# Kernel optimization log

Hardware: AMD Instinct MI355X
Metric: run time of the kernel (lower is better)

## Reference

```python
import jax, jax.numpy as jnp
import numpy as np

MODEL_DIM = 1024
NUM_HEADS = 8
DIM_PER_HEAD = MODEL_DIM // NUM_HEADS  # 128
BATCH = 4
NODE_LEN = 128  # must equal DIM_PER_HEAD (see v += relative_mul broadcast in source)
LN_EPS = 1e-5


def setup_inputs() -> dict:
    key0 = jax.random.key(0)
    ks = jax.random.split(key0, 16)
    def w(k, shape, s=0.02):
        return jax.random.normal(k, shape, dtype=jnp.float32) * s
    inp = {
        "key": jax.random.normal(ks[0], (BATCH, NODE_LEN, MODEL_DIM), dtype=jnp.float32),
        "value": jax.random.normal(ks[1], (BATCH, NODE_LEN, MODEL_DIM), dtype=jnp.float32),
        "query": jax.random.normal(ks[2], (BATCH, NODE_LEN, MODEL_DIM), dtype=jnp.float32),
        "relative_q": jax.random.normal(ks[3], (BATCH * NUM_HEADS, NODE_LEN, NODE_LEN, DIM_PER_HEAD), dtype=jnp.float32),
        "relative_v": jax.random.normal(ks[4], (BATCH * NUM_HEADS, NODE_LEN, NODE_LEN, DIM_PER_HEAD), dtype=jnp.float32),
        "Wq": w(ks[5], (MODEL_DIM, MODEL_DIM)), "bq": w(ks[6], (MODEL_DIM,)),
        "Wk": w(ks[7], (MODEL_DIM, MODEL_DIM)), "bk": w(ks[8], (MODEL_DIM,)),
        "Wv": w(ks[9], (MODEL_DIM, MODEL_DIM)), "bv": w(ks[10], (MODEL_DIM,)),
        "Wo": w(ks[11], (MODEL_DIM, MODEL_DIM)), "bo": w(ks[12], (MODEL_DIM,)),
        "ln_gamma": jnp.ones((MODEL_DIM,), dtype=jnp.float32),
        "ln_beta": jnp.zeros((MODEL_DIM,), dtype=jnp.float32),
    }
    return inp


def _relative_mul(x, rel):
    # x: [BH, L, d], rel: [BH, L, L, d] -> [BH, L, L]
    # result[b,i,j] = sum_d x[b,i,d] * rel[b,i,j,d]  (matches torch bmm chain)
    return jnp.einsum('bid,bijd->bij', x, rel)


def reference(key, value, query, relative_q, relative_v,
              Wq, bq, Wk, bk, Wv, bv, Wo, bo, ln_gamma, ln_beta):
    residual = query
    B = key.shape[0]
    H, d = NUM_HEADS, DIM_PER_HEAD

    k = key @ Wk.T + bk      # [B, L, model_dim]
    v = value @ Wv.T + bv
    q = query @ Wq.T + bq

    # faithful to torch .view(batch*heads, -1, dim_per_head): row-major reshape
    k = k.reshape(B * H, -1, d)  # [BH, L, d]
    v = v.reshape(B * H, -1, d)
    q = q.reshape(B * H, -1, d)

    # scale = (dim_per_head // num_heads) ** -0.5, as in source
    scale = (d // H) ** (-0.5)

    attn = jnp.einsum('bid,bjd->bij', q, k)           # [BH, L, L]
    attn = attn + _relative_mul(q, relative_q)
    attn = attn * scale
    attn = jax.nn.softmax(attn, axis=2)

    # source: v += relative_mul(v, relative_v); requires L == d
    v = v + _relative_mul(v, relative_v)              # [BH, L, d] (L == d)
    context = jnp.einsum('bij,bjd->bid', attn, v)     # [BH, L, d]
    context = context.reshape(B, -1, H * d)           # [B, L, model_dim]

    out = context @ Wo.T + bo
    out = out + residual
    mu = jnp.mean(out, axis=-1, keepdims=True)
    var = jnp.mean(jnp.square(out - mu), axis=-1, keepdims=True)
    out = (out - mu) * jax.lax.rsqrt(var + LN_EPS) * ln_gamma + ln_beta
    return (out, attn)
```

## Files before the change

kernel.cpp:

```cpp
#include <hip/hip_runtime.h>

#define MD 1024
#define L 128
#define LN_EPS 1e-5f

typedef __attribute__((ext_vector_type(8))) short bh8;
typedef __attribute__((ext_vector_type(4))) float fx4;
typedef __attribute__((ext_vector_type(4))) float f4;

__device__ __forceinline__ unsigned short f2bf(float x) {
  unsigned int u = __float_as_uint(x);
  u = (u + 0x7FFFu + ((u >> 16) & 1u)) >> 16;
  return (unsigned short)u;
}

__global__ __launch_bounds__(256) void cvt_bf16(
    const float* s0, const float* s1, const float* s2, const float* s3,
    const float* s4, const float* s5, const float* s6, unsigned short* d0,
    unsigned short* d1, unsigned short* d2, unsigned short* d3,
    unsigned short* d4, unsigned short* d5, unsigned short* d6) {
  const float* s;
  unsigned short* d;
  int n;
  switch (blockIdx.z) {
    case 0: s = s0; d = d0; n = 524288; break;
    case 1: s = s1; d = d1; n = 524288; break;
    case 2: s = s2; d = d2; n = 524288; break;
    case 3: s = s3; d = d3; n = 1048576; break;
    case 4: s = s4; d = d4; n = 1048576; break;
    case 5: s = s5; d = d5; n = 1048576; break;
    default: s = s6; d = d6; n = 1048576; break;
  }
  const int idx = (blockIdx.x * 256 + threadIdx.x) * 8;
  if (idx < n) {
    const float4 a = *(const float4*)&s[idx];
    const float4 b = *(const float4*)&s[idx + 4];
    uint4 o;
    o.x = (unsigned int)f2bf(a.x) | ((unsigned int)f2bf(a.y) << 16);
    o.y = (unsigned int)f2bf(a.z) | ((unsigned int)f2bf(a.w) << 16);
    o.z = (unsigned int)f2bf(b.x) | ((unsigned int)f2bf(b.y) << 16);
    o.w = (unsigned int)f2bf(b.z) | ((unsigned int)f2bf(b.w) << 16);
    *(uint4*)&d[idx] = o;
  }
}

__device__ __forceinline__ void mfma_gemm_body(
    const unsigned short* __restrict__ A, const unsigned short* __restrict__ W,
    const float* __restrict__ bias, float* __restrict__ out,
    unsigned short* __restrict__ outb) {
  __shared__ short As[64][40];
  __shared__ short Bs[64][40];
  const int t = threadIdx.x;
  const int row0 = blockIdx.x * 64;
  const int col0 = blockIdx.y * 64;
  const int l = t & 63;
  const int w = t >> 6;
  const int wr = (w >> 1) * 32;
  const int wc = (w & 1) * 32;
  const int srow = t >> 2;
  const int skg = (t & 3) * 8;
  const int fr = l & 15;
  const int fq = (l >> 4) * 8;

  fx4 z = {0.f, 0.f, 0.f, 0.f};
  fx4 acc[2][2];
  acc[0][0] = z; acc[0][1] = z; acc[1][0] = z; acc[1][1] = z;

  for (int k0 = 0; k0 < MD; k0 += 32) {
    const uint4 av = *(const uint4*)&A[(size_t)(row0 + srow) * MD + k0 + skg];
    const uint4 bv = *(const uint4*)&W[(size_t)(col0 + srow) * MD + k0 + skg];
    __syncthreads();
    *(uint4*)&As[srow][skg] = av;
    *(uint4*)&Bs[srow][skg] = bv;
    __syncthreads();
    const bh8 a0 = *(const bh8*)&As[wr + fr][fq];
    const bh8 a1 = *(const bh8*)&As[wr + 16 + fr][fq];
    const bh8 b0 = *(const bh8*)&Bs[wc + fr][fq];
    const bh8 b1 = *(const bh8*)&Bs[wc + 16 + fr][fq];
    acc[0][0] = __builtin_amdgcn_mfma_f32_16x16x32_bf16(a0, b0, acc[0][0], 0, 0, 0);
    acc[0][1] = __builtin_amdgcn_mfma_f32_16x16x32_bf16(a0, b1, acc[0][1], 0, 0, 0);
    acc[1][0] = __builtin_amdgcn_mfma_f32_16x16x32_bf16(a1, b0, acc[1][0], 0, 0, 0);
    acc[1][1] = __builtin_amdgcn_mfma_f32_16x16x32_bf16(a1, b1, acc[1][1], 0, 0, 0);
  }

  const int fq4 = (l >> 4) * 4;
#pragma unroll
  for (int m = 0; m < 2; m++)
#pragma unroll
    for (int n = 0; n < 2; n++) {
      const int col = col0 + wc + n * 16 + fr;
      const float bval = bias[col];
#pragma unroll
      for (int r = 0; r < 4; r++) {
        const int row = row0 + wr + m * 16 + fq4 + r;
        const float v = acc[m][n][r] + bval;
        if (out) out[(size_t)row * MD + col] = v;
        if (outb) outb[(size_t)row * MD + col] = f2bf(v);
      }
    }
}

__global__ __launch_bounds__(256) void qkv_mfma(
    const unsigned short* Aq, const unsigned short* Ak,
    const unsigned short* Av, const unsigned short* Wq,
    const unsigned short* Wk, const unsigned short* Wv, const float* bq,
    const float* bk, const float* bv, float* qo, float* ko, float* vo,
    unsigned short* qb, unsigned short* kb) {
  if (blockIdx.z == 0) mfma_gemm_body(Aq, Wq, bq, qo, qb);
  else if (blockIdx.z == 1) mfma_gemm_body(Ak, Wk, bk, ko, kb);
  else mfma_gemm_body(Av, Wv, bv, vo, nullptr);
}

__global__ __launch_bounds__(256) void o_mfma(const unsigned short* A,
                                              const unsigned short* W,
                                              const float* bias, float* out) {
  mfma_gemm_body(A, W, bias, out, nullptr);
}

__global__ __launch_bounds__(256) void qk_mfma(const unsigned short* __restrict__ qb,
                                               const unsigned short* __restrict__ kb,
                                               float* __restrict__ S1) {
  __shared__ short Qs[128][40];
  __shared__ short Ks[128][40];
  const int g = blockIdx.x;
  const int t = threadIdx.x;
  const int l = t & 63;
  const int w = t >> 6;
  const unsigned short* qg = qb + (size_t)g * 16384;
  const unsigned short* kg = kb + (size_t)g * 16384;
  const int srow = t >> 1;
  const int sh = (t & 1) * 16;
  const int fr = l & 15;
  const int fq = (l >> 4) * 8;

  fx4 z = {0.f, 0.f, 0.f, 0.f};
  fx4 acc[2][8];
#pragma unroll
  for (int m = 0; m < 2; m++)
#pragma unroll
    for (int n = 0; n < 8; n++) acc[m][n] = z;

  for (int d0 = 0; d0 < 128; d0 += 32) {
    const size_t off = (size_t)srow * 128 + d0 + sh;
    const uint4 q0 = *(const uint4*)&qg[off];
    const uint4 q1 = *(const uint4*)&qg[off + 8];
    const uint4 k0 = *(const uint4*)&kg[off];
    const uint4 k1 = *(const uint4*)&kg[off + 8];
    __syncthreads();
    *(uint4*)&Qs[srow][sh] = q0;
    *(uint4*)&Qs[srow][sh + 8] = q1;
    *(uint4*)&Ks[srow][sh] = k0;
    *(uint4*)&Ks[srow][sh + 8] = k1;
    __syncthreads();
    const bh8 a0 = *(const bh8*)&Qs[w * 32 + fr][fq];
    const bh8 a1 = *(const bh8*)&Qs[w * 32 + 16 + fr][fq];
#pragma unroll
    for (int n = 0; n < 8; n++) {
      const bh8 b = *(const bh8*)&Ks[n * 16 + fr][fq];
      acc[0][n] = __builtin_amdgcn_mfma_f32_16x16x32_bf16(a0, b, acc[0][n], 0, 0, 0);
      acc[1][n] = __builtin_amdgcn_mfma_f32_16x16x32_bf16(a1, b, acc[1][n], 0, 0, 0);
    }
  }

  const int fq4 = (l >> 4) * 4;
#pragma unroll
  for (int m = 0; m < 2; m++)
#pragma unroll
    for (int n = 0; n < 8; n++)
#pragma unroll
      for (int r = 0; r < 4; r++) {
        const int i = w * 32 + m * 16 + fq4 + r;
        S1[((size_t)g * 128 + i) * 128 + n * 16 + fr] = acc[m][n][r];
      }
}

__global__ __launch_bounds__(256) void rel_fused(
    const float* __restrict__ q, const float* __restrict__ v,
    const float* __restrict__ rq, const float* __restrict__ rv,
    const float* __restrict__ S1, float* __restrict__ attn,
    float* __restrict__ v2) {
  const int g = blockIdx.x;
  const int i = blockIdx.y;
  const int t = threadIdx.x;
  const int w = t >> 6;
  const int l = t & 63;
  const int c = t & 31;
  const int rlow = t >> 5;

  __shared__ float logits[L];
  __shared__ float vacc_s[L];

  const size_t gi = (size_t)g * L + i;
  const f4 qf = *(const f4*)&q[gi * 128 + c * 4];
  const f4 vf = *(const f4*)&v[gi * 128 + c * 4];

  const f4* rqp = (const f4*)(rq + gi * 16384);
  const f4* rvp = (const f4*)(rv + gi * 16384);

  float aq[16], av[16];
#pragma unroll
  for (int k = 0; k < 16; k++) {
    const f4 d = __builtin_nontemporal_load(&rqp[t + 256 * k]);
    aq[k] = qf.x * d.x + qf.y * d.y + qf.z * d.z + qf.w * d.w;
  }
#pragma unroll
  for (int k = 0; k < 16; k++) {
    const f4 d = __builtin_nontemporal_load(&rvp[t + 256 * k]);
    av[k] = vf.x * d.x + vf.y * d.y + vf.z * d.z + vf.w * d.w;
  }

#pragma unroll
  for (int mask = 1; mask <= 16; mask <<= 1) {
#pragma unroll
    for (int k = 0; k < 16; k++) {
      aq[k] += __shfl_xor(aq[k], mask);
      av[k] += __shfl_xor(av[k], mask);
    }
  }
  if (c == 0) {
#pragma unroll
    for (int k = 0; k < 16; k++) {
      const int row = 8 * k + rlow;
      logits[row] = aq[k];
      vacc_s[row] = av[k];
    }
  }

  __syncthreads();
  if (w == 0) {
    const float* S1p = S1 + gi * 128;
    const float x0 = (logits[l] + S1p[l]) * 0.25f;
    const float x1 = (logits[l + 64] + S1p[l + 64]) * 0.25f;
    float m = fmaxf(x0, x1);
#pragma unroll
    for (int mask = 1; mask <= 32; mask <<= 1) m = fmaxf(m, __shfl_xor(m, mask));
    const float e0 = __expf(x0 - m);
    const float e1 = __expf(x1 - m);
    float ssum = e0 + e1;
#pragma unroll
    for (int mask = 1; mask <= 32; mask <<= 1) ssum += __shfl_xor(ssum, mask);
    const float inv = 1.0f / ssum;
    attn[gi * 128 + l] = e0 * inv;
    attn[gi * 128 + l + 64] = e1 * inv;
  }
  if (t < 128) v2[gi * 128 + t] = v[gi * 128 + t] + vacc_s[t];
}

__global__ __launch_bounds__(256) void context_k(const float* __restrict__ attn,
                                                 const float* __restrict__ v2,
                                                 unsigned short* __restrict__ ctxb) {
  const int g = blockIdx.x;
  const int i = blockIdx.y;
  const int t = threadIdx.x;
  const int dd = t & 127;
  const int h = t >> 7;
  __shared__ float arow[L];
  __shared__ float part[128];
  const size_t gi = (size_t)g * L + i;
  if (t < L) arow[t] = attn[gi * 128 + t];
  __syncthreads();
  float acc = 0.f;
  const float* v2g = v2 + (size_t)g * (L * 128);
#pragma unroll 8
  for (int j = h * 64; j < h * 64 + 64; j++)
    acc = fmaf(arow[j], v2g[j * 128 + dd], acc);
  if (h == 1) part[dd] = acc;
  __syncthreads();
  if (h == 0) ctxb[gi * 128 + dd] = f2bf(acc + part[dd]);
}

__global__ __launch_bounds__(256) void resid_ln(const float* __restrict__ pre,
                                                const float* __restrict__ resid,
                                                const float* __restrict__ gamma,
                                                const float* __restrict__ beta,
                                                float* __restrict__ out) {
  const int r = blockIdx.x;
  const int t = threadIdx.x;
  const float4 p = *(const float4*)&pre[(size_t)r * MD + t * 4];
  const float4 rs = *(const float4*)&resid[(size_t)r * MD + t * 4];
  float4 x;
  x.x = p.x + rs.x; x.y = p.y + rs.y; x.z = p.z + rs.z; x.w = p.w + rs.w;
  float s = x.x + x.y + x.z + x.w;
  float ss = x.x * x.x + x.y * x.y + x.z * x.z + x.w * x.w;
#pragma unroll
  for (int mask = 1; mask <= 32; mask <<= 1) {
    s += __shfl_xor(s, mask);
    ss += __shfl_xor(ss, mask);
  }
  __shared__ float as_[4], aq_[4];
  const int w = t >> 6;
  if ((t & 63) == 0) { as_[w] = s; aq_[w] = ss; }
  __syncthreads();
  s = as_[0] + as_[1] + as_[2] + as_[3];
  ss = aq_[0] + aq_[1] + aq_[2] + aq_[3];
  const float mu = s * (1.0f / 1024.0f);
  const float var = ss * (1.0f / 1024.0f) - mu * mu;
  const float inv = rsqrtf(var + LN_EPS);
  const float4 g4 = *(const float4*)&gamma[t * 4];
  const float4 b4 = *(const float4*)&beta[t * 4];
  float4 o;
  o.x = (x.x - mu) * inv * g4.x + b4.x;
  o.y = (x.y - mu) * inv * g4.y + b4.y;
  o.z = (x.z - mu) * inv * g4.z + b4.z;
  o.w = (x.w - mu) * inv * g4.w + b4.w;
  *(float4*)&out[(size_t)r * MD + t * 4] = o;
}

extern "C" void kernel_launch(void* const* d_in, const int* in_sizes, int n_in,
                              void* d_out, int out_size, void* d_ws,
                              size_t ws_size, hipStream_t stream) {
  (void)in_sizes; (void)n_in; (void)out_size; (void)ws_size;
  const float* key = (const float*)d_in[0];
  const float* value = (const float*)d_in[1];
  const float* query = (const float*)d_in[2];
  const float* rq = (const float*)d_in[3];
  const float* rv = (const float*)d_in[4];
  const float* Wq = (const float*)d_in[5];
  const float* bq = (const float*)d_in[6];
  const float* Wk = (const float*)d_in[7];
  const float* bk = (const float*)d_in[8];
  const float* Wv = (const float*)d_in[9];
  const float* bv = (const float*)d_in[10];
  const float* Wo = (const float*)d_in[11];
  const float* bo = (const float*)d_in[12];
  const float* gamma = (const float*)d_in[13];
  const float* beta = (const float*)d_in[14];

  float* out0 = (float*)d_out;
  float* attn_out = (float*)d_out + 524288;

  float* ws = (float*)d_ws;
  float* q_ws = ws;
  float* k_ws = ws + 524288;
  float* v_ws = ws + 2 * 524288;
  float* v2_ws = ws + 3 * 524288;
  float* pre_ws = ws + 4 * 524288;
  float* S1_ws = ws + 5 * 524288;
  unsigned short* us = (unsigned short*)(ws + 6 * 524288);
  unsigned short* qb = us;
  unsigned short* kb = us + 524288;
  unsigned short* inqb = us + 2 * 524288;
  unsigned short* inkb = us + 3 * 524288;
  unsigned short* invb = us + 4 * 524288;
  unsigned short* ctxb = us + 5 * 524288;
  unsigned short* Wqb = us + 6 * 524288;
  unsigned short* Wkb = Wqb + 1048576;
  unsigned short* Wvb = Wkb + 1048576;
  unsigned short* Wob = Wvb + 1048576;

  cvt_bf16<<<dim3(512, 1, 7), 256, 0, stream>>>(query, key, value, Wq, Wk, Wv,
                                                Wo, inqb, inkb, invb, Wqb, Wkb,
                                                Wvb, Wob);
  qkv_mfma<<<dim3(8, 16, 3), 256, 0, stream>>>(inqb, inkb, invb, Wqb, Wkb, Wvb,
                                               bq, bk, bv, q_ws, k_ws, v_ws,
                                               qb, kb);
  qk_mfma<<<32, 256, 0, stream>>>(qb, kb, S1_ws);
  rel_fused<<<dim3(32, 128), 256, 0, stream>>>(q_ws, v_ws, rq, rv, S1_ws,
                                               attn_out, v2_ws);
  context_k<<<dim3(32, 128), 256, 0, stream>>>(attn_out, v2_ws, ctxb);
  o_mfma<<<dim3(8, 16), 256, 0, stream>>>(ctxb, Wob, bo, pre_ws);
  resid_ln<<<512, 256, 0, stream>>>(pre_ws, query, gamma, beta, out0);
}
```

Baseline: 150.8 us.

## Fuse bf16 conversion into GEMM loads and compute context with MFMA

Removes the separate fp32-to-bf16 conversion kernel by converting inputs and weights on the fly inside the GEMM tile loads. Drops the unused fp32 k output. The attention-times-V product moves from a scalar FMA kernel to a bf16 MFMA kernel; rel_fused now emits a bf16 copy of attn and a transposed bf16 v2. GEMM loads now read twice the bytes per tile, and the context product loses precision in bf16. The new MFMA context kernel launches only 32 blocks, so parallelism is low.

```diff
diff --git a/kernel.cpp b/kernel.cpp
--- a/kernel.cpp
+++ b/kernel.cpp
@@ -14,38 +14,18 @@
   return (unsigned short)u;
 }
 
-__global__ __launch_bounds__(256) void cvt_bf16(
-    const float* s0, const float* s1, const float* s2, const float* s3,
-    const float* s4, const float* s5, const float* s6, unsigned short* d0,
-    unsigned short* d1, unsigned short* d2, unsigned short* d3,
-    unsigned short* d4, unsigned short* d5, unsigned short* d6) {
-  const float* s;
-  unsigned short* d;
-  int n;
-  switch (blockIdx.z) {
-    case 0: s = s0; d = d0; n = 524288; break;
-    case 1: s = s1; d = d1; n = 524288; break;
-    case 2: s = s2; d = d2; n = 524288; break;
-    case 3: s = s3; d = d3; n = 1048576; break;
-    case 4: s = s4; d = d4; n = 1048576; break;
-    case 5: s = s5; d = d5; n = 1048576; break;
-    default: s = s6; d = d6; n = 1048576; break;
-  }
-  const int idx = (blockIdx.x * 256 + threadIdx.x) * 8;
-  if (idx < n) {
-    const float4 a = *(const float4*)&s[idx];
-    const float4 b = *(const float4*)&s[idx + 4];
-    uint4 o;
-    o.x = (unsigned int)f2bf(a.x) | ((unsigned int)f2bf(a.y) << 16);
-    o.y = (unsigned int)f2bf(a.z) | ((unsigned int)f2bf(a.w) << 16);
-    o.z = (unsigned int)f2bf(b.x) | ((unsigned int)f2bf(b.y) << 16);
-    o.w = (unsigned int)f2bf(b.z) | ((unsigned int)f2bf(b.w) << 16);
-    *(uint4*)&d[idx] = o;
-  }
-}
-
+__device__ __forceinline__ uint4 pack8(const float4 a, const float4 b) {
+  uint4 o;
+  o.x = (unsigned int)f2bf(a.x) | ((unsigned int)f2bf(a.y) << 16);
+  o.y = (unsigned int)f2bf(a.z) | ((unsigned int)f2bf(a.w) << 16);
+  o.z = (unsigned int)f2bf(b.x) | ((unsigned int)f2bf(b.y) << 16);
+  o.w = (unsigned int)f2bf(b.z) | ((unsigned int)f2bf(b.w) << 16);
+  return o;
+}
+
+template <int AMODE>
 __device__ __forceinline__ void mfma_gemm_body(
-    const unsigned short* __restrict__ A, const unsigned short* __restrict__ W,
+    const void* __restrict__ Ap, const float* __restrict__ Wf,
     const float* __restrict__ bias, float* __restrict__ out,
     unsigned short* __restrict__ outb) {
   __shared__ short As[64][40];
@@ -67,8 +47,21 @@
   acc[0][0] = z; acc[0][1] = z; acc[1][0] = z; acc[1][1] = z;
 
   for (int k0 = 0; k0 < MD; k0 += 32) {
-    const uint4 av = *(const uint4*)&A[(size_t)(row0 + srow) * MD + k0 + skg];
-    const uint4 bv = *(const uint4*)&W[(size_t)(col0 + srow) * MD + k0 + skg];
+    uint4 av, bv;
+    if (AMODE == 1) {
+      const unsigned short* Ab = (const unsigned short*)Ap;
+      av = *(const uint4*)&Ab[(size_t)(row0 + srow) * MD + k0 + skg];
+    } else {
+      const float* Af = (const float*)Ap;
+      const float4 a0 = *(const float4*)&Af[(size_t)(row0 + srow) * MD + k0 + skg];
+      const float4 a1 = *(const float4*)&Af[(size_t)(row0 + srow) * MD + k0 + skg + 4];
+      av = pack8(a0, a1);
+    }
+    {
+      const float4 b0 = *(const float4*)&Wf[(size_t)(col0 + srow) * MD + k0 + skg];
+      const float4 b1 = *(const float4*)&Wf[(size_t)(col0 + srow) * MD + k0 + skg + 4];
+      bv = pack8(b0, b1);
+    }
     __syncthreads();
     *(uint4*)&As[srow][skg] = av;
     *(uint4*)&Bs[srow][skg] = bv;
@@ -101,20 +94,19 @@
 }
 
 __global__ __launch_bounds__(256) void qkv_mfma(
-    const unsigned short* Aq, const unsigned short* Ak,
-    const unsigned short* Av, const unsigned short* Wq,
-    const unsigned short* Wk, const unsigned short* Wv, const float* bq,
-    const float* bk, const float* bv, float* qo, float* ko, float* vo,
+    const float* query, const float* key, const float* value,
+    const float* Wq, const float* Wk, const float* Wv, const float* bq,
+    const float* bk, const float* bv, float* qo, float* vo,
     unsigned short* qb, unsigned short* kb) {
-  if (blockIdx.z == 0) mfma_gemm_body(Aq, Wq, bq, qo, qb);
-  else if (blockIdx.z == 1) mfma_gemm_body(Ak, Wk, bk, ko, kb);
-  else mfma_gemm_body(Av, Wv, bv, vo, nullptr);
+  if (blockIdx.z == 0) mfma_gemm_body<0>(query, Wq, bq, qo, qb);
+  else if (blockIdx.z == 1) mfma_gemm_body<0>(key, Wk, bk, nullptr, kb);
+  else mfma_gemm_body<0>(value, Wv, bv, vo, nullptr);
 }
 
 __global__ __launch_bounds__(256) void o_mfma(const unsigned short* A,
-                                              const unsigned short* W,
+                                              const float* W,
                                               const float* bias, float* out) {
-  mfma_gemm_body(A, W, bias, out, nullptr);
+  mfma_gemm_body<1>(A, W, bias, out, nullptr);
 }
 
 __global__ __launch_bounds__(256) void qk_mfma(const unsigned short* __restrict__ qb,
@@ -178,7 +170,7 @@
     const float* __restrict__ q, const float* __restrict__ v,
     const float* __restrict__ rq, const float* __restrict__ rv,
     const float* __restrict__ S1, float* __restrict__ attn,
-    float* __restrict__ v2) {
+    unsigned short* __restrict__ attnb, unsigned short* __restrict__ v2tb) {
   const int g = blockIdx.x;
   const int i = blockIdx.y;
   const int t = threadIdx.x;
@@ -240,33 +232,76 @@
 #pragma unroll
     for (int mask = 1; mask <= 32; mask <<= 1) ssum += __shfl_xor(ssum, mask);
     const float inv = 1.0f / ssum;
-    attn[gi * 128 + l] = e0 * inv;
-    attn[gi * 128 + l + 64] = e1 * inv;
-  }
-  if (t < 128) v2[gi * 128 + t] = v[gi * 128 + t] + vacc_s[t];
-}
-
-__global__ __launch_bounds__(256) void context_k(const float* __restrict__ attn,
-                                                 const float* __restrict__ v2,
-                                                 unsigned short* __restrict__ ctxb) {
+    const float a0 = e0 * inv;
+    const float a1 = e1 * inv;
+    attn[gi * 128 + l] = a0;
+    attn[gi * 128 + l + 64] = a1;
+    attnb[gi * 128 + l] = f2bf(a0);
+    attnb[gi * 128 + l + 64] = f2bf(a1);
+  }
+  if (t < 128) {
+    const float val = v[gi * 128 + t] + vacc_s[t];
+    v2tb[(size_t)g * 16384 + (size_t)t * 128 + i] = f2bf(val);
+  }
+}
+
+__global__ __launch_bounds__(256) void ctx_mfma(
+    const unsigned short* __restrict__ attnb,
+    const unsigned short* __restrict__ v2tb,
+    unsigned short* __restrict__ ctxb) {
+  __shared__ short Qs[128][40];
+  __shared__ short Ks[128][40];
   const int g = blockIdx.x;
-  const int i = blockIdx.y;
-  const int t = threadIdx.x;
-  const int dd = t & 127;
-  const int h = t >> 7;
-  __shared__ float arow[L];
-  __shared__ float part[128];
-  const size_t gi = (size_t)g * L + i;
-  if (t < L) arow[t] = attn[gi * 128 + t];
-  __syncthreads();
-  float acc = 0.f;
-  const float* v2g = v2 + (size_t)g * (L * 128);
-#pragma unroll 8
-  for (int j = h * 64; j < h * 64 + 64; j++)
-    acc = fmaf(arow[j], v2g[j * 128 + dd], acc);
-  if (h == 1) part[dd] = acc;
-  __syncthreads();
-  if (h == 0) ctxb[gi * 128 + dd] = f2bf(acc + part[dd]);
+  const int t = threadIdx.x;
+  const int l = t & 63;
+  const int w = t >> 6;
+  const unsigned short* ag = attnb + (size_t)g * 16384;
+  const unsigned short* bg = v2tb + (size_t)g * 16384;
+  const int srow = t >> 1;
+  const int sh = (t & 1) * 16;
+  const int fr = l & 15;
+  const int fq = (l >> 4) * 8;
+
+  fx4 z = {0.f, 0.f, 0.f, 0.f};
+  fx4 acc[2][8];
+#pragma unroll
+  for (int m = 0; m < 2; m++)
+#pragma unroll
+    for (int n = 0; n < 8; n++) acc[m][n] = z;
+
+  for (int j0 = 0; j0 < 128; j0 += 32) {
+    const size_t off = (size_t)srow * 128 + j0 + sh;
+    const uint4 q0 = *(const uint4*)&ag[off];
+    const uint4 q1 = *(const uint4*)&ag[off + 8];
+    const uint4 k0 = *(const uint4*)&bg[off];
+    const uint4 k1 = *(const uint4*)&bg[off + 8];
+    __syncthreads();
+    *(uint4*)&Qs[srow][sh] = q0;
+    *(uint4*)&Qs[srow][sh + 8] = q1;
+    *(uint4*)&Ks[srow][sh] = k0;
+    *(uint4*)&Ks[srow][sh + 8] = k1;
+    __syncthreads();
+    const bh8 a0 = *(const bh8*)&Qs[w * 32 + fr][fq];
+    const bh8 a1 = *(const bh8*)&Qs[w * 32 + 16 + fr][fq];
+#pragma unroll
+    for (int n = 0; n < 8; n++) {
+      const bh8 b = *(const bh8*)&Ks[n * 16 + fr][fq];
+      acc[0][n] = __builtin_amdgcn_mfma_f32_16x16x32_bf16(a0, b, acc[0][n], 0, 0, 0);
+      acc[1][n] = __builtin_amdgcn_mfma_f32_16x16x32_bf16(a1, b, acc[1][n], 0, 0, 0);
+    }
+  }
+
+  const int fq4 = (l >> 4) * 4;
+#pragma unroll
+  for (int m = 0; m < 2; m++)
+#pragma unroll
+    for (int n = 0; n < 8; n++)
+#pragma unroll
+      for (int r = 0; r < 4; r++) {
+        const int i = w * 32 + m * 16 + fq4 + r;
+        ctxb[(size_t)g * 16384 + (size_t)i * 128 + n * 16 + fr] =
+            f2bf(acc[m][n][r]);
+      }
 }
 
 __global__ __launch_bounds__(256) void resid_ln(const float* __restrict__ pre,
@@ -331,33 +366,22 @@
 
   float* ws = (float*)d_ws;
   float* q_ws = ws;
-  float* k_ws = ws + 524288;
-  float* v_ws = ws + 2 * 524288;
-  float* v2_ws = ws + 3 * 524288;
-  float* pre_ws = ws + 4 * 524288;
-  float* S1_ws = ws + 5 * 524288;
-  unsigned short* us = (unsigned short*)(ws + 6 * 524288);
+  float* v_ws = ws + 524288;
+  float* pre_ws = ws + 2 * 524288;
+  float* S1_ws = ws + 3 * 524288;
+  unsigned short* us = (unsigned short*)(ws + 4 * 524288);
   unsigned short* qb = us;
   unsigned short* kb = us + 524288;
-  unsigned short* inqb = us + 2 * 524288;
-  unsigned short* inkb = us + 3 * 524288;
-  unsigned short* invb = us + 4 * 524288;
-  unsigned short* ctxb = us + 5 * 524288;
-  unsigned short* Wqb = us + 6 * 524288;
-  unsigned short* Wkb = Wqb + 1048576;
-  unsigned short* Wvb = Wkb + 1048576;
-  unsigned short* Wob = Wvb + 1048576;
-
-  cvt_bf16<<<dim3(512, 1, 7), 256, 0, stream>>>(query, key, value, Wq, Wk, Wv,
-                                                Wo, inqb, inkb, invb, Wqb, Wkb,
-                                                Wvb, Wob);
-  qkv_mfma<<<dim3(8, 16, 3), 256, 0, stream>>>(inqb, inkb, invb, Wqb, Wkb, Wvb,
-                                               bq, bk, bv, q_ws, k_ws, v_ws,
-                                               qb, kb);
+  unsigned short* attnb = us + 2 * 524288;
+  unsigned short* v2tb = us + 3 * 524288;
+  unsigned short* ctxb = us + 4 * 524288;
+
+  qkv_mfma<<<dim3(8, 16, 3), 256, 0, stream>>>(query, key, value, Wq, Wk, Wv,
+                                               bq, bk, bv, q_ws, v_ws, qb, kb);
   qk_mfma<<<32, 256, 0, stream>>>(qb, kb, S1_ws);
   rel_fused<<<dim3(32, 128), 256, 0, stream>>>(q_ws, v_ws, rq, rv, S1_ws,
-                                               attn_out, v2_ws);
-  context_k<<<dim3(32, 128), 256, 0, stream>>>(attn_out, v2_ws, ctxb);
-  o_mfma<<<dim3(8, 16), 256, 0, stream>>>(ctxb, Wob, bo, pre_ws);
+                                               attn_out, attnb, v2tb);
+  ctx_mfma<<<32, 256, 0, stream>>>(attnb, v2tb, ctxb);
+  o_mfma<<<dim3(8, 16), 256, 0, stream>>>(ctxb, Wo, bo, pre_ws);
   resid_ln<<<512, 256, 0, stream>>>(pre_ws, query, gamma, beta, out0);
 }
```

Result: slower. 161.2 us (+6.8%).
